# Optimization experiments

Hardware: AMD Instinct MI355X
Metric: run time of the kernel (lower is better)

## Reference

```python
import jax, jax.numpy as jnp
import numpy as np

NUM_EXPERTS = 8
HIDDEN = 2048
INTER = 4096
TOKENS = 8192
TOP_K = 2


def setup_inputs() -> dict:
    key = jax.random.key(0)
    ks = jax.random.split(key, 5)
    s = 0.02
    return {
        "x": jax.random.normal(ks[0], (TOKENS, HIDDEN), dtype=jnp.float32),
        "gate_w": jax.random.normal(ks[1], (NUM_EXPERTS, HIDDEN), dtype=jnp.float32) * s,
        "w1": jax.random.normal(ks[2], (NUM_EXPERTS, INTER, HIDDEN), dtype=jnp.float32) * s,
        "w2": jax.random.normal(ks[3], (NUM_EXPERTS, HIDDEN, INTER), dtype=jnp.float32) * s,
        "w3": jax.random.normal(ks[4], (NUM_EXPERTS, INTER, HIDDEN), dtype=jnp.float32) * s,
    }


def reference(x, gate_w, w1, w2, w3):
    # Router: softmax over experts in fp32, then top-2 (no renormalization,
    # matching the torch module which uses the raw top-k softmax probs).
    router_logits = jnp.einsum("th,eh->te", x, gate_w)  # [T, E]
    probs = jax.nn.softmax(router_logits.astype(jnp.float32), axis=1)
    topk_w, topk_idx = jax.lax.top_k(probs, TOP_K)  # [T, K]
    topk_w = topk_w.astype(x.dtype)

    num_experts = w1.shape[0]
    out = jnp.zeros_like(x)
    for e in range(num_experts):
        # Combined routing coefficient for expert e per token (0 if unrouted).
        coef = jnp.sum(jnp.where(topk_idx == e, topk_w, 0.0), axis=1)  # [T]
        # SwiGLU expert FFN: down(silu(gate(x)) * up(x))
        g = jnp.einsum("th,ih->ti", x, w1[e])
        u = jnp.einsum("th,ih->ti", x, w3[e])
        h = jax.nn.silu(g) * u
        y = jnp.einsum("ti,hi->th", h, w2[e])
        out = out + coef[:, None] * y
    return out
```

## Files before the change

kernel.cpp:

```cpp
#include <hip/hip_runtime.h>
#include <stdint.h>
#include <stddef.h>


constexpr int kTokens  = 8192;
constexpr int kHidden  = 2048;
constexpr int kInter   = 4096;
constexpr int kExperts = 8;

constexpr int BM = 128, BN = 128, BK = 64;
constexpr int MAX_MT = (2 * kTokens) / BM + kExperts;
constexpr int NTY = kInter / BK;
constexpr int kSlotCap = 16512;
constexpr int GU_BLOCKS = (kInter / BN) * MAX_MT;

typedef short bf16x8 __attribute__((ext_vector_type(8)));
typedef float f32x4  __attribute__((ext_vector_type(4)));
typedef unsigned int u32;

__device__ __forceinline__ unsigned short f2bf(float f) {
  union { float f; unsigned u; } v; v.f = f;
  unsigned r = v.u + 0x7FFFu + ((v.u >> 16) & 1u);
  return (unsigned short)(r >> 16);
}

__device__ __forceinline__ void gload16(const void* g, void* l) {
  __builtin_amdgcn_global_load_lds(
      (const __attribute__((address_space(1))) u32*)g,
      (__attribute__((address_space(3))) u32*)l, 16, 0, 0);
}

__device__ __forceinline__ void convert_body(
    const float* __restrict__ src, unsigned short* __restrict__ dst,
    int lp, int lq, int K, long nchunks, int bid, int nblocks)
{
  long stride = (long)nblocks * 256;
  for (long g = bid * 256L + threadIdx.x; g < nchunks; g += stride) {
    int  l   = (int)(g & 1023);
    long blk = g >> 10;
    int  q   = (int)(blk & ((1 << lq) - 1));
    long ep  = blk >> lq;
    int  p   = (int)(ep & ((1 << lp) - 1));
    int  e   = (int)(ep >> lp);
    int r = l >> 3, cs = l & 7, c = cs ^ (r & 7);
    size_t soff = (((size_t)(e << lp) + p) * 128 + r) * (size_t)K + (size_t)q * 64 + c * 8;
    float4 v0 = *reinterpret_cast<const float4*>(src + soff);
    float4 v1 = *reinterpret_cast<const float4*>(src + soff + 4);
    uint4 o;
    o.x = (u32)f2bf(v0.x) | ((u32)f2bf(v0.y) << 16);
    o.y = (u32)f2bf(v0.z) | ((u32)f2bf(v0.w) << 16);
    o.z = (u32)f2bf(v1.x) | ((u32)f2bf(v1.y) << 16);
    o.w = (u32)f2bf(v1.z) | ((u32)f2bf(v1.w) << 16);
    *reinterpret_cast<uint4*>(dst + g * 8) = o;
  }
}

__global__ __launch_bounds__(256) void convert_w(
    const float* __restrict__ src, unsigned short* __restrict__ dst,
    int lp, int lq, int K, long nchunks)
{
  convert_body(src, dst, lp, lq, K, nchunks, blockIdx.x, gridDim.x);
}

__device__ __forceinline__ void router_body(
    const float* __restrict__ x, const float* __restrict__ gate_w,
    unsigned short* __restrict__ xb, int* __restrict__ counts,
    int* __restrict__ list_idx, float* __restrict__ list_w, int bid)
{
  const int lane = threadIdx.x & 63;
  const int wave = threadIdx.x >> 6;
  const int t = bid * 4 + wave;

  float acc[kExperts];
#pragma unroll
  for (int e = 0; e < kExperts; ++e) acc[e] = 0.f;

  const float4* xrow = reinterpret_cast<const float4*>(x + (size_t)t * kHidden);
#pragma unroll
  for (int j = 0; j < 8; ++j) {
    float4 xv = xrow[j * 64 + lane];
    uint2 pk;
    pk.x = (u32)f2bf(xv.x) | ((u32)f2bf(xv.y) << 16);
    pk.y = (u32)f2bf(xv.z) | ((u32)f2bf(xv.w) << 16);
    *reinterpret_cast<uint2*>(xb + (size_t)t * kHidden + j * 256 + lane * 4) = pk;
#pragma unroll
    for (int e = 0; e < kExperts; ++e) {
      float4 gv = reinterpret_cast<const float4*>(gate_w + (size_t)e * kHidden)[j * 64 + lane];
      acc[e] += xv.x * gv.x + xv.y * gv.y + xv.z * gv.z + xv.w * gv.w;
    }
  }
#pragma unroll
  for (int e = 0; e < kExperts; ++e) {
#pragma unroll
    for (int m = 32; m >= 1; m >>= 1) acc[e] += __shfl_xor(acc[e], m);
  }
  if (lane == 0) {
    float mx = acc[0];
#pragma unroll
    for (int e = 1; e < kExperts; ++e) mx = fmaxf(mx, acc[e]);
    float p[kExperts]; float s = 0.f;
#pragma unroll
    for (int e = 0; e < kExperts; ++e) { p[e] = __expf(acc[e] - mx); s += p[e]; }
    float inv = 1.f / s;
    int i1 = 0; float v1 = p[0];
#pragma unroll
    for (int e = 1; e < kExperts; ++e) if (p[e] > v1) { v1 = p[e]; i1 = e; }
    int i2 = (i1 == 0) ? 1 : 0; float v2 = p[i2];
#pragma unroll
    for (int e = 0; e < kExperts; ++e) {
      if (e == i1 || e == i2) continue;
      if (p[e] > v2) { v2 = p[e]; i2 = e; }
    }
    int s1 = atomicAdd(&counts[i1], 1);
    list_idx[i1 * kTokens + s1] = t * 2 + 0;
    list_w [i1 * kTokens + s1] = v1 * inv;
    int s2 = atomicAdd(&counts[i2], 1);
    list_idx[i2 * kTokens + s2] = t * 2 + 1;
    list_w [i2 * kTokens + s2] = v2 * inv;
  }
}

__global__ __launch_bounds__(256) void moe_prep(
    const float* __restrict__ x, const float* __restrict__ gate_w,
    unsigned short* __restrict__ xb, int* __restrict__ counts,
    int* __restrict__ list_idx, float* __restrict__ list_w,
    const float* __restrict__ w1, unsigned short* __restrict__ w1b,
    const float* __restrict__ w3, unsigned short* __restrict__ w3b,
    long nchunks)
{
  const int bid = blockIdx.x;
  if (bid < 2048) {
    router_body(x, gate_w, xb, counts, list_idx, list_w, bid);
  } else if (bid < 2048 + 4096) {
    convert_body(w1, w1b, 5, 5, kHidden, nchunks, bid - 2048, 4096);
  } else {
    convert_body(w3, w3b, 5, 5, kHidden, nchunks, bid - 6144, 4096);
  }
}

__global__ __launch_bounds__(256) void moe_router(
    const float* __restrict__ x, const float* __restrict__ gate_w,
    unsigned short* __restrict__ xb, int* __restrict__ counts,
    int* __restrict__ list_idx, float* __restrict__ list_w)
{
  router_body(x, gate_w, xb, counts, list_idx, list_w, blockIdx.x);
}

__device__ __forceinline__ bool map_tile(const int* __restrict__ counts, int mt,
                                         int& e, int& lm, int& sb, int& ne)
{
  int tb = 0; sb = 0;
  for (e = 0; e < kExperts; ++e) {
    ne = counts[e];
    int tiles = (ne + BM - 1) / BM;
    if (mt < tb + tiles) { lm = mt - tb; return true; }
    tb += tiles; sb += ne;
  }
  return false;
}

__device__ __forceinline__ void gu_body(
    const unsigned short* __restrict__ xb,
    const unsigned short* __restrict__ w1b, const unsigned short* __restrict__ w3b,
    const int* __restrict__ counts, const int* __restrict__ list_idx,
    unsigned short* __restrict__ hbuf, int bid)
{
  __shared__ unsigned short As [BM * BK];
  __shared__ unsigned short B1s[BN * BK];
  __shared__ unsigned short B3s[BN * BK];
  __shared__ int toks[BM];

  const int tid = threadIdx.x;
  const int nt  = bid / MAX_MT;
  const int mt  = bid % MAX_MT;

  int e, lm, sb, ne;
  if (!map_tile(counts, mt, e, lm, sb, ne)) return;
  const int row0 = lm * BM;

  if (tid < BM) {
    int lr = row0 + tid;
    toks[tid] = list_idx[e * kTokens + ((lr < ne) ? lr : 0)] >> 1;
  }
  __syncthreads();

  const int lane = tid & 63;
  const int w = tid >> 6;
  const int wr = w >> 1, wc = w & 1;

  const unsigned short* srcA[4];
  const unsigned short* srcB1[4];
  const unsigned short* srcB3[4];
  const size_t bbase = ((size_t)(e * (kInter / BN) + nt) * (kHidden / BK)) * 1024;
#pragma unroll
  for (int i = 0; i < 4; ++i) {
    int l = (w * 4 + i) * 64 + lane;
    int r = l >> 3, cs = l & 7, c = cs ^ (r & 7);
    srcA[i]  = xb  + (size_t)toks[r] * kHidden + c * 8;
    srcB1[i] = w1b + (bbase + l) * 8;
    srcB3[i] = w3b + (bbase + l) * 8;
  }

  f32x4 accG[4][4], accU[4][4];
  const f32x4 zero = {0.f, 0.f, 0.f, 0.f};
#pragma unroll
  for (int m = 0; m < 4; ++m)
#pragma unroll
    for (int n = 0; n < 4; ++n) { accG[m][n] = zero; accU[m][n] = zero; }

  for (int ks = 0; ks < kHidden / BK; ++ks) {
#pragma unroll
    for (int i = 0; i < 4; ++i) {
      gload16(srcA[i]  + ks * BK,            &As [(w * 4 + i) * 512]);
      gload16(srcB1[i] + (size_t)ks * 8192,  &B1s[(w * 4 + i) * 512]);
      gload16(srcB3[i] + (size_t)ks * 8192,  &B3s[(w * 4 + i) * 512]);
    }
    __syncthreads();
#pragma unroll
    for (int kk = 0; kk < 2; ++kk) {
      const int cq = kk * 4 + (lane >> 4);
      bf16x8 a[4], b1v[4], b3v[4];
#pragma unroll
      for (int m = 0; m < 4; ++m) {
        int row = wr * 64 + m * 16 + (lane & 15);
        a[m] = *reinterpret_cast<const bf16x8*>(&As[row * 64 + ((cq ^ (row & 7)) << 3)]);
      }
#pragma unroll
      for (int n = 0; n < 4; ++n) {
        int row = wc * 64 + n * 16 + (lane & 15);
        b1v[n] = *reinterpret_cast<const bf16x8*>(&B1s[row * 64 + ((cq ^ (row & 7)) << 3)]);
        b3v[n] = *reinterpret_cast<const bf16x8*>(&B3s[row * 64 + ((cq ^ (row & 7)) << 3)]);
      }
#pragma unroll
      for (int m = 0; m < 4; ++m)
#pragma unroll
        for (int n = 0; n < 4; ++n) {
          accG[m][n] = __builtin_amdgcn_mfma_f32_16x16x32_bf16(a[m], b1v[n], accG[m][n], 0, 0, 0);
          accU[m][n] = __builtin_amdgcn_mfma_f32_16x16x32_bf16(a[m], b3v[n], accU[m][n], 0, 0, 0);
        }
    }
    __syncthreads();
  }

#pragma unroll
  for (int m = 0; m < 4; ++m) {
#pragma unroll
    for (int r = 0; r < 4; ++r) {
      int rloc = wr * 64 + m * 16 + ((lane >> 4) * 4) + r;
      int lrow = row0 + rloc;
      if (lrow < ne) {
        size_t base = (size_t)(sb + lrow) * kInter + (size_t)nt * BN + wc * 64 + (lane & 15);
#pragma unroll
        for (int n = 0; n < 4; ++n) {
          float g = accG[m][n][r];
          float u = accU[m][n][r];
          float hv = (g / (1.f + __expf(-g))) * u;
          hbuf[base + n * 16] = f2bf(hv);
        }
      }
    }
  }
}

__global__ __launch_bounds__(256, 2) void moe_gu(
    const unsigned short* __restrict__ xb,
    const unsigned short* __restrict__ w1b, const unsigned short* __restrict__ w3b,
    const int* __restrict__ counts, const int* __restrict__ list_idx,
    unsigned short* __restrict__ hbuf)
{
  gu_body(xb, w1b, w3b, counts, list_idx, hbuf, blockIdx.x);
}

__global__ __launch_bounds__(256, 2) void moe_gu_fused(
    const unsigned short* __restrict__ xb,
    const unsigned short* __restrict__ w1b, const unsigned short* __restrict__ w3b,
    const int* __restrict__ counts, const int* __restrict__ list_idx,
    unsigned short* __restrict__ hbuf,
    const float* __restrict__ w2, unsigned short* __restrict__ w2b, long nch)
{
  const int bid = blockIdx.x;
  if (bid < GU_BLOCKS) {
    gu_body(xb, w1b, w3b, counts, list_idx, hbuf, bid);
  } else {
    convert_body(w2, w2b, 4, 6, kInter, nch, bid - GU_BLOCKS, 4096);
  }
}

__global__ __launch_bounds__(256, 2) void moe_y9(
    const unsigned short* __restrict__ hbuf,
    const unsigned short* __restrict__ w2b,
    const int* __restrict__ counts, const int* __restrict__ list_idx,
    const float* __restrict__ list_w,
    unsigned short* __restrict__ ybuf16)
{
  __shared__ unsigned short As[BM * BK];
  __shared__ unsigned short Bs[2][128 * BK];
  __shared__ int   toks[BM];
  __shared__ float cofs[BM];
  __shared__ int   rnks[BM];

  const int tid = threadIdx.x;
  const int grp = blockIdx.x / MAX_MT;
  const int mt  = blockIdx.x % MAX_MT;
  const int ks  = grp >> 3;
  const int nt  = grp & 7;

  int e, lm, sb, ne;
  if (!map_tile(counts, mt, e, lm, sb, ne)) return;
  const int row0 = lm * BM;

  if (tid < BM) {
    int lr = row0 + tid;
    bool v = lr < ne;
    int pk = v ? list_idx[e * kTokens + lr] : 0;
    toks[tid] = pk >> 1;
    rnks[tid] = pk & 1;
    cofs[tid] = v ? list_w[e * kTokens + lr] : 0.f;
  }
  __syncthreads();

  const int lane = tid & 63;
  const int w    = tid >> 6;

  const unsigned short* srcA[4];
  int cOffB[4];
#pragma unroll
  for (int i = 0; i < 4; ++i) {
    int l = (w * 4 + i) * 64 + lane;
    int r = l >> 3, c = (l & 7) ^ (r & 7);
    int rg = sb + row0 + r;
    if (rg > kSlotCap - 1) rg = kSlotCap - 1;
    srcA[i] = hbuf + (size_t)rg * kInter + c * 8;
    cOffB[i] = l * 8;
  }
  const unsigned short* pB[2];
#pragma unroll
  for (int h = 0; h < 2; ++h)
    pB[h] = w2b + (size_t)(e * 16 + nt * 2 + h) * NTY * 8192;

  f32x4 acc[8][4];
  const f32x4 zero = {0.f, 0.f, 0.f, 0.f};
#pragma unroll
  for (int m = 0; m < 8; ++m)
#pragma unroll
    for (int n = 0; n < 4; ++n) acc[m][n] = zero;

  const int bh  = w >> 1;
  const int br0 = (w & 1) * 64;

  const int kt0 = ks * (NTY / 2);
  for (int kt = kt0; kt < kt0 + NTY / 2; ++kt) {
#pragma unroll
    for (int i = 0; i < 4; ++i) {
      gload16(srcA[i] + kt * BK,                   &As   [(w * 4 + i) * 512]);
      gload16(pB[0] + (size_t)kt * 8192 + cOffB[i], &Bs[0][(w * 4 + i) * 512]);
      gload16(pB[1] + (size_t)kt * 8192 + cOffB[i], &Bs[1][(w * 4 + i) * 512]);
    }
    __syncthreads();
#pragma unroll
    for (int kk = 0; kk < 2; ++kk) {
      const int cq = kk * 4 + (lane >> 4);
      bf16x8 a[8], b[4];
#pragma unroll
      for (int m = 0; m < 8; ++m) {
        int row = m * 16 + (lane & 15);
        a[m] = *reinterpret_cast<const bf16x8*>(&As[row * 64 + ((cq ^ (row & 7)) << 3)]);
      }
#pragma unroll
      for (int n = 0; n < 4; ++n) {
        int rl = br0 + n * 16 + (lane & 15);
        b[n] = *reinterpret_cast<const bf16x8*>(&Bs[bh][rl * 64 + ((cq ^ (rl & 7)) << 3)]);
      }
#pragma unroll
      for (int m = 0; m < 8; ++m)
#pragma unroll
        for (int n = 0; n < 4; ++n)
          acc[m][n] = __builtin_amdgcn_mfma_f32_16x16x32_bf16(a[m], b[n], acc[m][n], 0, 0, 0);
    }
    __syncthreads();
  }

#pragma unroll
  for (int m = 0; m < 8; ++m) {
#pragma unroll
    for (int r = 0; r < 4; ++r) {
      int rloc = m * 16 + ((lane >> 4) * 4) + r;
      if (row0 + rloc < ne) {
        float cf = cofs[rloc];
        size_t obase = ((size_t)(rnks[rloc] * 2 + ks) * kTokens + toks[rloc]) * kHidden
                     + (size_t)nt * 256 + w * 64 + (lane & 15);
#pragma unroll
        for (int n = 0; n < 4; ++n)
          ybuf16[obase + n * 16] = f2bf(cf * acc[m][n][r]);
      }
    }
  }
}

__global__ __launch_bounds__(256) void moe_merge4(
    const unsigned short* __restrict__ yb, float* __restrict__ out, long n8)
{
  const size_t bs = (size_t)kTokens * kHidden;
  long stride = (long)gridDim.x * blockDim.x;
  for (long i = blockIdx.x * (long)blockDim.x + threadIdx.x; i < n8; i += stride) {
    float s[8];
#pragma unroll
    for (int k = 0; k < 8; ++k) s[k] = 0.f;
#pragma unroll
    for (int b = 0; b < 4; ++b) {
      uint4 v = *reinterpret_cast<const uint4*>(yb + b * bs + (size_t)i * 8);
      const unsigned short* h = reinterpret_cast<const unsigned short*>(&v);
#pragma unroll
      for (int k = 0; k < 8; ++k) {
        union { unsigned u; float f; } cv; cv.u = (unsigned)h[k] << 16;
        s[k] += cv.f;
      }
    }
    float4 o0 = {s[0], s[1], s[2], s[3]};
    float4 o1 = {s[4], s[5], s[6], s[7]};
    *reinterpret_cast<float4*>(out + (size_t)i * 8)     = o0;
    *reinterpret_cast<float4*>(out + (size_t)i * 8 + 4) = o1;
  }
}

__global__ __launch_bounds__(256, 2) void moe_gu_f32(
    const unsigned short* __restrict__ xb,
    const float* __restrict__ w1, const float* __restrict__ w3,
    const int* __restrict__ counts, const int* __restrict__ list_idx,
    unsigned short* __restrict__ hbuf)
{
  __shared__ unsigned short As [BM * BK];
  __shared__ unsigned short B1s[BN * BK];
  __shared__ unsigned short B3s[BN * BK];
  __shared__ int toks[BM];

  const int tid = threadIdx.x;
  const int nt  = blockIdx.x / MAX_MT;
  const int mt  = blockIdx.x % MAX_MT;

  int e, lm, sb, ne;
  if (!map_tile(counts, mt, e, lm, sb, ne)) return;
  const int row0 = lm * BM;

  if (tid < BM) {
    int lr = row0 + tid;
    toks[tid] = list_idx[e * kTokens + ((lr < ne) ? lr : 0)] >> 1;
  }
  __syncthreads();

  const unsigned short* aptr[4];
#pragma unroll
  for (int i = 0; i < 4; ++i) {
    int chunk = i * 256 + tid;
    int r = chunk >> 3, c8 = chunk & 7;
    aptr[i] = xb + (size_t)toks[r] * kHidden + c8 * 8;
  }
  const float* w1e = w1 + (size_t)e * kInter * kHidden;
  const float* w3e = w3 + (size_t)e * kInter * kHidden;

  f32x4 accG[4][4], accU[4][4];
  const f32x4 zero = {0.f, 0.f, 0.f, 0.f};
#pragma unroll
  for (int m = 0; m < 4; ++m)
#pragma unroll
    for (int n = 0; n < 4; ++n) { accG[m][n] = zero; accU[m][n] = zero; }

  const int lane = tid & 63;
  const int wr = (tid >> 6) >> 1;
  const int wc = (tid >> 6) & 1;

  for (int k0 = 0; k0 < kHidden; k0 += BK) {
#pragma unroll
    for (int i = 0; i < 4; ++i) {
      int chunk = i * 256 + tid;
      uint4 v = *reinterpret_cast<const uint4*>(aptr[i] + k0);
      *reinterpret_cast<uint4*>(&As[chunk * 8]) = v;
    }
#pragma unroll
    for (int i = 0; i < 8; ++i) {
      int c = i * 256 + tid;
      int rowB = c >> 4, c16 = c & 15;
      size_t off = ((size_t)(nt * BN + rowB)) * kHidden + k0 + c16 * 4;
      float4 v1 = *reinterpret_cast<const float4*>(w1e + off);
      float4 v3 = *reinterpret_cast<const float4*>(w3e + off);
      uint2 p1, p3;
      p1.x = (u32)f2bf(v1.x) | ((u32)f2bf(v1.y) << 16);
      p1.y = (u32)f2bf(v1.z) | ((u32)f2bf(v1.w) << 16);
      p3.x = (u32)f2bf(v3.x) | ((u32)f2bf(v3.y) << 16);
      p3.y = (u32)f2bf(v3.z) | ((u32)f2bf(v3.w) << 16);
      *reinterpret_cast<uint2*>(&B1s[rowB * BK + c16 * 4]) = p1;
      *reinterpret_cast<uint2*>(&B3s[rowB * BK + c16 * 4]) = p3;
    }
    __syncthreads();
#pragma unroll
    for (int kk = 0; kk < 2; ++kk) {
      const int klo = kk * 32 + (lane >> 4) * 8;
      bf16x8 a[4], b1v[4], b3v[4];
#pragma unroll
      for (int m = 0; m < 4; ++m)
        a[m] = *reinterpret_cast<const bf16x8*>(&As[(wr * 64 + m * 16 + (lane & 15)) * BK + klo]);
#pragma unroll
      for (int n = 0; n < 4; ++n) {
        b1v[n] = *reinterpret_cast<const bf16x8*>(&B1s[(wc * 64 + n * 16 + (lane & 15)) * BK + klo]);
        b3v[n] = *reinterpret_cast<const bf16x8*>(&B3s[(wc * 64 + n * 16 + (lane & 15)) * BK + klo]);
      }
#pragma unroll
      for (int m = 0; m < 4; ++m)
#pragma unroll
        for (int n = 0; n < 4; ++n) {
          accG[m][n] = __builtin_amdgcn_mfma_f32_16x16x32_bf16(a[m], b1v[n], accG[m][n], 0, 0, 0);
          accU[m][n] = __builtin_amdgcn_mfma_f32_16x16x32_bf16(a[m], b3v[n], accU[m][n], 0, 0, 0);
        }
    }
    __syncthreads();
  }
#pragma unroll
  for (int m = 0; m < 4; ++m) {
#pragma unroll
    for (int r = 0; r < 4; ++r) {
      int rloc = wr * 64 + m * 16 + ((lane >> 4) * 4) + r;
      int lrow = row0 + rloc;
      if (lrow < ne) {
        size_t base = (size_t)(sb + lrow) * kInter + (size_t)nt * BN + wc * 64 + (lane & 15);
#pragma unroll
        for (int n = 0; n < 4; ++n) {
          float g = accG[m][n][r];
          float u = accU[m][n][r];
          hbuf[base + n * 16] = f2bf((g / (1.f + __expf(-g))) * u);
        }
      }
    }
  }
}

__global__ __launch_bounds__(256, 2) void moe_y_f32(
    const unsigned short* __restrict__ hbuf,
    const float* __restrict__ w2,
    const int* __restrict__ counts, const int* __restrict__ list_idx,
    const float* __restrict__ list_w,
    float* __restrict__ out)
{
  __shared__ unsigned short As[BM * BK];
  __shared__ unsigned short Bs[BN * BK];
  __shared__ int   toks[BM];
  __shared__ float cofs[BM];

  const int tid = threadIdx.x;
  const int nt  = blockIdx.x / MAX_MT;
  const int mt  = blockIdx.x % MAX_MT;

  int e, lm, sb, ne;
  if (!map_tile(counts, mt, e, lm, sb, ne)) return;
  const int row0 = lm * BM;

  if (tid < BM) {
    int lr = row0 + tid;
    bool v = lr < ne;
    toks[tid] = v ? (list_idx[e * kTokens + lr] >> 1) : 0;
    cofs[tid] = v ? list_w [e * kTokens + lr] : 0.f;
  }
  __syncthreads();

  const float* w2e = w2 + (size_t)e * kHidden * kInter;
  const unsigned short* arow = hbuf + (size_t)(sb + row0) * kInter;

  f32x4 acc[4][4];
  const f32x4 zero = {0.f, 0.f, 0.f, 0.f};
#pragma unroll
  for (int m = 0; m < 4; ++m)
#pragma unroll
    for (int n = 0; n < 4; ++n) acc[m][n] = zero;

  const int lane = tid & 63;
  const int wr = (tid >> 6) >> 1;
  const int wc = (tid >> 6) & 1;

  for (int k0 = 0; k0 < kInter; k0 += BK) {
#pragma unroll
    for (int i = 0; i < 4; ++i) {
      int chunk = i * 256 + tid;
      int r = chunk >> 3, c8 = chunk & 7;
      uint4 v = *reinterpret_cast<const uint4*>(arow + (size_t)r * kInter + k0 + c8 * 8);
      *reinterpret_cast<uint4*>(&As[chunk * 8]) = v;
    }
#pragma unroll
    for (int i = 0; i < 8; ++i) {
      int c = i * 256 + tid;
      int rowB = c >> 4, c16 = c & 15;
      size_t off = ((size_t)(nt * BN + rowB)) * kInter + k0 + c16 * 4;
      float4 v2 = *reinterpret_cast<const float4*>(w2e + off);
      uint2 p2;
      p2.x = (u32)f2bf(v2.x) | ((u32)f2bf(v2.y) << 16);
      p2.y = (u32)f2bf(v2.z) | ((u32)f2bf(v2.w) << 16);
      *reinterpret_cast<uint2*>(&Bs[rowB * BK + c16 * 4]) = p2;
    }
    __syncthreads();
#pragma unroll
    for (int kk = 0; kk < 2; ++kk) {
      const int klo = kk * 32 + (lane >> 4) * 8;
      bf16x8 a[4], b[4];
#pragma unroll
      for (int m = 0; m < 4; ++m)
        a[m] = *reinterpret_cast<const bf16x8*>(&As[(wr * 64 + m * 16 + (lane & 15)) * BK + klo]);
#pragma unroll
      for (int n = 0; n < 4; ++n)
        b[n] = *reinterpret_cast<const bf16x8*>(&Bs[(wc * 64 + n * 16 + (lane & 15)) * BK + klo]);
#pragma unroll
      for (int m = 0; m < 4; ++m)
#pragma unroll
        for (int n = 0; n < 4; ++n)
          acc[m][n] = __builtin_amdgcn_mfma_f32_16x16x32_bf16(a[m], b[n], acc[m][n], 0, 0, 0);
    }
    __syncthreads();
  }
#pragma unroll
  for (int m = 0; m < 4; ++m) {
#pragma unroll
    for (int r = 0; r < 4; ++r) {
      int rloc = wr * 64 + m * 16 + ((lane >> 4) * 4) + r;
      if (row0 + rloc < ne) {
        float cf = cofs[rloc];
        size_t obase = (size_t)toks[rloc] * kHidden + (size_t)nt * BN + wc * 64 + (lane & 15);
#pragma unroll
        for (int n = 0; n < 4; ++n)
          atomicAdd(&out[obase + n * 16], cf * acc[m][n][r]);
      }
    }
  }
}

extern "C" void kernel_launch(void* const* d_in, const int* in_sizes, int n_in,
                              void* d_out, int out_size, void* d_ws, size_t ws_size,
                              hipStream_t stream)
{
  const float* x      = (const float*)d_in[0];
  const float* gate_w = (const float*)d_in[1];
  const float* w1     = (const float*)d_in[2];
  const float* w2     = (const float*)d_in[3];
  const float* w3     = (const float*)d_in[4];
  float* out = (float*)d_out;

  char* ws = (char*)d_ws;
  const size_t MiB = 1ull << 20;
  int*   counts   = (int*)(ws);
  int*   list_idx = (int*)(ws + 1024);
  float* list_w   = (float*)(ws + 1024 + kExperts * kTokens * 4);

  hipMemsetAsync(counts, 0, 1024, stream);

  const long nch = (long)kExperts * 32 * 32 * 1024;

  if (ws_size >= 547 * MiB) {
    unsigned short* xb     = (unsigned short*)(ws + 1 * MiB);
    unsigned short* w1b    = (unsigned short*)(ws + 33 * MiB);
    unsigned short* w3b    = (unsigned short*)(ws + 161 * MiB);
    unsigned short* hbuf   = (unsigned short*)(ws + 289 * MiB);
    unsigned short* w2b    = (unsigned short*)(ws + 418 * MiB);
    unsigned short* ybuf16 = (unsigned short*)(ws + 161 * MiB);

    moe_prep<<<10240, 256, 0, stream>>>(x, gate_w, xb, counts, list_idx, list_w,
                                        w1, w1b, w3, w3b, nch);
    moe_gu_fused<<<GU_BLOCKS + 4096, 256, 0, stream>>>(
        xb, w1b, w3b, counts, list_idx, hbuf, w2, w2b, nch);
    moe_y9<<<16 * MAX_MT, 256, 0, stream>>>(hbuf, w2b, counts, list_idx, list_w, ybuf16);
    moe_merge4<<<2048, 256, 0, stream>>>(ybuf16, out, (long)kTokens * kHidden / 8);
  } else if (ws_size >= 418 * MiB) {
    unsigned short* xb     = (unsigned short*)(ws + 1 * MiB);
    unsigned short* w1b    = (unsigned short*)(ws + 33 * MiB);
    unsigned short* w3b    = (unsigned short*)(ws + 161 * MiB);
    unsigned short* hbuf   = (unsigned short*)(ws + 289 * MiB);
    unsigned short* w2b    = w1b;
    unsigned short* ybuf16 = (unsigned short*)(ws + 161 * MiB);

    moe_prep<<<10240, 256, 0, stream>>>(x, gate_w, xb, counts, list_idx, list_w,
                                        w1, w1b, w3, w3b, nch);
    moe_gu<<<GU_BLOCKS, 256, 0, stream>>>(xb, w1b, w3b, counts, list_idx, hbuf);
    convert_w<<<4096, 256, 0, stream>>>(w2, w2b, 4, 6, kInter, nch);
    moe_y9<<<16 * MAX_MT, 256, 0, stream>>>(hbuf, w2b, counts, list_idx, list_w, ybuf16);
    moe_merge4<<<2048, 256, 0, stream>>>(ybuf16, out, (long)kTokens * kHidden / 8);
  } else {
    unsigned short* xb   = (unsigned short*)(ws + 1 * MiB);
    unsigned short* hbuf = (unsigned short*)(ws + 36 * MiB);
    hipMemsetAsync(out, 0, (size_t)kTokens * kHidden * sizeof(float), stream);
    moe_router<<<kTokens / 4, 256, 0, stream>>>(x, gate_w, xb, counts, list_idx, list_w);
    moe_gu_f32<<<(kInter / BN) * MAX_MT, 256, 0, stream>>>(xb, w1, w3, counts, list_idx, hbuf);
    moe_y_f32 <<<(kHidden / BN) * MAX_MT, 256, 0, stream>>>(hbuf, w2, counts, list_idx, list_w, out);
  }
}
```

Measured before the change: 1.402 ms.

## Widen down-projection tiles to 512 columns with 512-thread blocks and 4-way split-K

```diff
diff --git a/kernel.cpp b/kernel.cpp
--- a/kernel.cpp
+++ b/kernel.cpp
@@ -286,7 +286,7 @@
   }
 }
 
-__global__ __launch_bounds__(256, 2) void moe_y9(
+__global__ __launch_bounds__(512, 2) void moe_y10(
     const unsigned short* __restrict__ hbuf,
     const unsigned short* __restrict__ w2b,
     const int* __restrict__ counts, const int* __restrict__ list_idx,
@@ -294,7 +294,7 @@
     unsigned short* __restrict__ ybuf16)
 {
   __shared__ unsigned short As[BM * BK];
-  __shared__ unsigned short Bs[2][128 * BK];
+  __shared__ unsigned short Bs[4][128 * BK];
   __shared__ int   toks[BM];
   __shared__ float cofs[BM];
   __shared__ int   rnks[BM];
@@ -302,8 +302,8 @@
   const int tid = threadIdx.x;
   const int grp = blockIdx.x / MAX_MT;
   const int mt  = blockIdx.x % MAX_MT;
-  const int ks  = grp >> 3;
-  const int nt  = grp & 7;
+  const int ks  = grp >> 2;
+  const int nt  = grp & 3;
 
   int e, lm, sb, ne;
   if (!map_tile(counts, mt, e, lm, sb, ne)) return;
@@ -322,6 +322,121 @@
   const int lane = tid & 63;
   const int w    = tid >> 6;
 
+  const unsigned short* srcA[2];
+  int cOffB[2];
+#pragma unroll
+  for (int j = 0; j < 2; ++j) {
+    int l = (w * 2 + j) * 64 + lane;
+    int r = l >> 3, c = (l & 7) ^ (r & 7);
+    int rg = sb + row0 + r;
+    if (rg > kSlotCap - 1) rg = kSlotCap - 1;
+    srcA[j] = hbuf + (size_t)rg * kInter + c * 8;
+    cOffB[j] = l * 8;
+  }
+  const unsigned short* pB[4];
+#pragma unroll
+  for (int h = 0; h < 4; ++h)
+    pB[h] = w2b + (size_t)(e * 16 + nt * 4 + h) * NTY * 8192;
+
+  f32x4 acc[8][4];
+  const f32x4 zero = {0.f, 0.f, 0.f, 0.f};
+#pragma unroll
+  for (int m = 0; m < 8; ++m)
+#pragma unroll
+    for (int n = 0; n < 4; ++n) acc[m][n] = zero;
+
+  const int ph  = w >> 1;
+  const int br0 = (w & 1) * 64;
+
+  const int kt0 = ks * (NTY / 4);
+  for (int kt = kt0; kt < kt0 + NTY / 4; ++kt) {
+#pragma unroll
+    for (int j = 0; j < 2; ++j) {
+      gload16(srcA[j] + kt * BK, &As[(w * 2 + j) * 512]);
+#pragma unroll
+      for (int h = 0; h < 4; ++h)
+        gload16(pB[h] + (size_t)kt * 8192 + cOffB[j], &Bs[h][(w * 2 + j) * 512]);
+    }
+    __syncthreads();
+#pragma unroll
+    for (int kk = 0; kk < 2; ++kk) {
+      const int cq = kk * 4 + (lane >> 4);
+      bf16x8 a[8], b[4];
+#pragma unroll
+      for (int m = 0; m < 8; ++m) {
+        int row = m * 16 + (lane & 15);
+        a[m] = *reinterpret_cast<const bf16x8*>(&As[row * 64 + ((cq ^ (row & 7)) << 3)]);
+      }
+#pragma unroll
+      for (int n = 0; n < 4; ++n) {
+        int rl = br0 + n * 16 + (lane & 15);
+        b[n] = *reinterpret_cast<const bf16x8*>(&Bs[ph][rl * 64 + ((cq ^ (rl & 7)) << 3)]);
+      }
+#pragma unroll
+      for (int m = 0; m < 8; ++m)
+#pragma unroll
+        for (int n = 0; n < 4; ++n)
+          acc[m][n] = __builtin_amdgcn_mfma_f32_16x16x32_bf16(a[m], b[n], acc[m][n], 0, 0, 0);
+    }
+    __syncthreads();
+  }
+
+#pragma unroll
+  for (int m = 0; m < 8; ++m) {
+#pragma unroll
+    for (int r = 0; r < 4; ++r) {
+      int rloc = m * 16 + ((lane >> 4) * 4) + r;
+      if (row0 + rloc < ne) {
+        float cf = cofs[rloc];
+        size_t obase = ((size_t)(rnks[rloc] * 4 + ks) * kTokens + toks[rloc]) * kHidden
+                     + (size_t)nt * 512 + (ph * 128 + br0) + ((lane & 15) - br0) + br0
+                     ;
+        obase = ((size_t)(rnks[rloc] * 4 + ks) * kTokens + toks[rloc]) * kHidden
+              + (size_t)nt * 512 + w * 64 + (lane & 15);
+#pragma unroll
+        for (int n = 0; n < 4; ++n)
+          ybuf16[obase + n * 16] = f2bf(cf * acc[m][n][r]);
+      }
+    }
+  }
+}
+
+__global__ __launch_bounds__(256, 2) void moe_y9(
+    const unsigned short* __restrict__ hbuf,
+    const unsigned short* __restrict__ w2b,
+    const int* __restrict__ counts, const int* __restrict__ list_idx,
+    const float* __restrict__ list_w,
+    unsigned short* __restrict__ ybuf16)
+{
+  __shared__ unsigned short As[BM * BK];
+  __shared__ unsigned short Bs[2][128 * BK];
+  __shared__ int   toks[BM];
+  __shared__ float cofs[BM];
+  __shared__ int   rnks[BM];
+
+  const int tid = threadIdx.x;
+  const int grp = blockIdx.x / MAX_MT;
+  const int mt  = blockIdx.x % MAX_MT;
+  const int ks  = grp >> 3;
+  const int nt  = grp & 7;
+
+  int e, lm, sb, ne;
+  if (!map_tile(counts, mt, e, lm, sb, ne)) return;
+  const int row0 = lm * BM;
+
+  if (tid < BM) {
+    int lr = row0 + tid;
+    bool v = lr < ne;
+    int pk = v ? list_idx[e * kTokens + lr] : 0;
+    toks[tid] = pk >> 1;
+    rnks[tid] = pk & 1;
+    cofs[tid] = v ? list_w[e * kTokens + lr] : 0.f;
+  }
+  __syncthreads();
+
+  const int lane = tid & 63;
+  const int w    = tid >> 6;
+
   const unsigned short* srcA[4];
   int cOffB[4];
 #pragma unroll
@@ -408,6 +523,32 @@
     for (int k = 0; k < 8; ++k) s[k] = 0.f;
 #pragma unroll
     for (int b = 0; b < 4; ++b) {
+      uint4 v = *reinterpret_cast<const uint4*>(yb + b * bs + (size_t)i * 8);
+      const unsigned short* h = reinterpret_cast<const unsigned short*>(&v);
+#pragma unroll
+      for (int k = 0; k < 8; ++k) {
+        union { unsigned u; float f; } cv; cv.u = (unsigned)h[k] << 16;
+        s[k] += cv.f;
+      }
+    }
+    float4 o0 = {s[0], s[1], s[2], s[3]};
+    float4 o1 = {s[4], s[5], s[6], s[7]};
+    *reinterpret_cast<float4*>(out + (size_t)i * 8)     = o0;
+    *reinterpret_cast<float4*>(out + (size_t)i * 8 + 4) = o1;
+  }
+}
+
+__global__ __launch_bounds__(256) void moe_merge8(
+    const unsigned short* __restrict__ yb, float* __restrict__ out, long n8)
+{
+  const size_t bs = (size_t)kTokens * kHidden;
+  long stride = (long)gridDim.x * blockDim.x;
+  for (long i = blockIdx.x * (long)blockDim.x + threadIdx.x; i < n8; i += stride) {
+    float s[8];
+#pragma unroll
+    for (int k = 0; k < 8; ++k) s[k] = 0.f;
+#pragma unroll
+    for (int b = 0; b < 8; ++b) {
       uint4 v = *reinterpret_cast<const uint4*>(yb + b * bs + (size_t)i * 8);
       const unsigned short* h = reinterpret_cast<const unsigned short*>(&v);
 #pragma unroll
@@ -656,14 +797,14 @@
     unsigned short* w3b    = (unsigned short*)(ws + 161 * MiB);
     unsigned short* hbuf   = (unsigned short*)(ws + 289 * MiB);
     unsigned short* w2b    = (unsigned short*)(ws + 418 * MiB);
-    unsigned short* ybuf16 = (unsigned short*)(ws + 161 * MiB);
+    unsigned short* ybuf16 = (unsigned short*)(ws + 33 * MiB);
 
     moe_prep<<<10240, 256, 0, stream>>>(x, gate_w, xb, counts, list_idx, list_w,
                                         w1, w1b, w3, w3b, nch);
     moe_gu_fused<<<GU_BLOCKS + 4096, 256, 0, stream>>>(
         xb, w1b, w3b, counts, list_idx, hbuf, w2, w2b, nch);
-    moe_y9<<<16 * MAX_MT, 256, 0, stream>>>(hbuf, w2b, counts, list_idx, list_w, ybuf16);
-    moe_merge4<<<2048, 256, 0, stream>>>(ybuf16, out, (long)kTokens * kHidden / 8);
+    moe_y10<<<16 * MAX_MT, 512, 0, stream>>>(hbuf, w2b, counts, list_idx, list_w, ybuf16);
+    moe_merge8<<<2048, 256, 0, stream>>>(ybuf16, out, (long)kTokens * kHidden / 8);
   } else if (ws_size >= 418 * MiB) {
     unsigned short* xb     = (unsigned short*)(ws + 1 * MiB);
     unsigned short* w1b    = (unsigned short*)(ws + 33 * MiB);
```

Measured after the change: 1.545 ms. 1.1x slower.
